# Kernel tuning notes

Hardware: AMD Instinct MI355X
Metric: run time of the kernel (lower is better)

## Reference

```python
import jax, jax.numpy as jnp
import numpy as np

K_HEADS = 8
D_HEAD = 16
D_MODEL = K_HEADS * D_HEAD  # 128


def _xavier(key, shape):
    fan_in, fan_out = shape[0], shape[1]
    limit = (6.0 / (fan_in + fan_out)) ** 0.5
    return jax.random.uniform(key, shape, jnp.float32, -limit, limit)


def setup_inputs() -> dict:
    key = jax.random.key(0)
    ks = jax.random.split(key, 8)
    B, T, N = 8, 12, 512
    X = jax.random.normal(ks[0], (B, T, N, D_MODEL), jnp.float32)
    STE = jax.random.normal(ks[1], (B, T, N, 2 * D_MODEL), jnp.float32)
    Wq = _xavier(ks[2], (3 * D_MODEL, D_MODEL))
    Wk = _xavier(ks[3], (3 * D_MODEL, D_MODEL))
    Wv = _xavier(ks[4], (3 * D_MODEL, D_MODEL))
    Wo = _xavier(ks[5], (D_MODEL, D_MODEL))
    bq = jnp.zeros((D_MODEL,), jnp.float32)
    bk = jnp.zeros((D_MODEL,), jnp.float32)
    bv = jnp.zeros((D_MODEL,), jnp.float32)
    bo = jnp.zeros((D_MODEL,), jnp.float32)
    return {"X": X, "STE": STE, "Wq": Wq, "bq": bq, "Wk": Wk, "bk": bk,
            "Wv": Wv, "bv": bv, "Wo": Wo, "bo": bo}


def reference(X, STE, Wq, bq, Wk, bk, Wv, bv, Wo, bo):
    # 1x1-conv FCs == per-(t,node) linear + relu on the last dim
    H = jnp.concatenate([X, STE], axis=-1)              # [B,T,N,3D]
    q = jax.nn.relu(H @ Wq + bq)                        # [B,T,N,D]
    k = jax.nn.relu(H @ Wk + bk)
    v = jax.nn.relu(H @ Wv + bv)
    B, T, N, D = q.shape

    def heads(x):  # split last dim into K heads (head index major), move to front
        return x.reshape(B, T, N, K_HEADS, D_HEAD).transpose(3, 0, 1, 2, 4)

    qh, kh, vh = heads(q), heads(k), heads(v)           # [K,B,T,N,d]
    att = jnp.einsum('kbtnd,kbtmd->kbtnm', qh, kh) / (D_HEAD ** 0.5)
    att = jax.nn.softmax(att, axis=-1)                  # [K,B,T,N,N]
    o = jnp.einsum('kbtnm,kbtmd->kbtnd', att, vh)       # [K,B,T,N,d]
    o = o.transpose(1, 2, 3, 0, 4).reshape(B, T, N, D)  # concat heads on last dim
    return jax.nn.relu(o @ Wo + bo)
```

## Files before the change

kernel.cpp:

```cpp
#include <hip/hip_runtime.h>
#include <math.h>

constexpr int B_  = 8;
constexpr int T_  = 12;
constexpr int N_  = 512;
constexpr int DM  = 128;
constexpr int KH  = 8;
constexpr int DH  = 16;
constexpr int MR  = B_*T_*N_;
constexpr int K3  = 3*DM;
constexpr int TB  = 256;

typedef __attribute__((ext_vector_type(8))) short  bf16x8;
typedef __attribute__((ext_vector_type(4))) float  f32x4;
typedef __attribute__((ext_vector_type(4))) int    i32x4;

#define LOG2E 1.44269504088896340736f
#define SHIFT2 28.8539008177792681f

static __device__ inline float fast_exp2(float x) {
#if __has_builtin(__builtin_amdgcn_exp2f)
    return __builtin_amdgcn_exp2f(x);
#else
    return __expf(0.69314718055994531f * x);
#endif
}

static __device__ inline unsigned short f2bf(float x) {
    unsigned u = __float_as_uint(x);
    return (unsigned short)((u + 0x7fffu + ((u >> 16) & 1u)) >> 16);
}
static __device__ inline unsigned pk2(float a, float b) {
    unsigned ua = __float_as_uint(a) + 0x8000u;
    unsigned ub = __float_as_uint(b) + 0x8000u;
    return __builtin_amdgcn_perm(ub, ua, 0x07060302u);
}
static __device__ inline unsigned pk2t(float a, float b) {
    return __builtin_amdgcn_perm(__float_as_uint(b), __float_as_uint(a),
                                 0x07060302u);
}
static __device__ inline float fast_rcp(float x) {
#if __has_builtin(__builtin_amdgcn_rcpf)
    return __builtin_amdgcn_rcpf(x);
#else
    return 1.0f / x;
#endif
}

__global__ __launch_bounds__(256) void wprep_kernel(
    const float* __restrict__ Wq, const float* __restrict__ Wk,
    const float* __restrict__ Wv, const float* __restrict__ Wo,
    unsigned short* __restrict__ Wfrag, unsigned short* __restrict__ Wot)
{
    const int idx = blockIdx.x*256 + threadIdx.x;
    if (idx < 3*K3*DM) {
        const int p   = idx / (K3*DM);
        const int rem = idx - p*(K3*DM);
        const int k   = rem >> 7;
        const int n   = rem & 127;
        const float* W = (p == 0) ? Wq : ((p == 1) ? Wk : Wv);
        const int c   = p*DM + n;
        const int nb  = c >> 4, mm = c & 15;
        const int ktI = k >> 6, kr = k & 63;
        const int ksI = kr >> 5, gg = (kr >> 3) & 3, ee = kr & 7;
        Wfrag[(((ktI*24 + nb)*2 + ksI) << 9) + ((gg*16 + mm) << 3) + ee]
            = f2bf(W[rem]);
    } else {
        const int i2 = idx - 3*K3*DM;
        const int k  = i2 >> 7;
        const int n  = i2 & 127;
        Wot[n*DM + k] = f2bf(Wo[i2]);
    }
}

__global__ __launch_bounds__(256, 4) void qkv_fused(
    const float* __restrict__ X, const float* __restrict__ STE,
    const unsigned short* __restrict__ Wfrag,
    const float* __restrict__ bq, const float* __restrict__ bk,
    const float* __restrict__ bv,
    unsigned short* __restrict__ qb, unsigned short* __restrict__ kb2,
    unsigned short* __restrict__ vb2)
{
    __shared__ __align__(16) unsigned short Ash[2][64*72];
    const int tid = threadIdx.x;
    const int rb  = blockIdx.x * 64;
    const int ch  = blockIdx.y;

    const int lane = tid & 63, wv = tid >> 6;
    const int m15 = lane & 15, g = lane >> 4;

    const int ar  = tid >> 4;
    const int ac4 = (tid & 15) * 4;

    float4 a0, a1, a2, a3;

#define QF_LOADA(kt_) {                                                      \
        const float* __restrict__ asrc = ((kt_) < DM) ? (X + (kt_))          \
                                                      : (STE + ((kt_) - DM));\
        const int ldr = ((kt_) < DM) ? DM : 2*DM;                            \
        const float* __restrict__ ap = asrc + (size_t)(rb + ar)*ldr + ac4;   \
        a0 = *(const float4*)(ap           );                                \
        a1 = *(const float4*)(ap + 16*ldr  );                                \
        a2 = *(const float4*)(ap + 32*ldr  );                                \
        a3 = *(const float4*)(ap + 48*ldr  ); }

#define QF_STOREA(buf_) {                                                    \
        unsigned short* Aw = Ash[buf_] + ar*72 + ac4;                        \
        uint2 d;                                                             \
        d.x = pk2(a0.x, a0.y); d.y = pk2(a0.z, a0.w); *(uint2*)(Aw        ) = d; \
        d.x = pk2(a1.x, a1.y); d.y = pk2(a1.z, a1.w); *(uint2*)(Aw + 16*72) = d; \
        d.x = pk2(a2.x, a2.y); d.y = pk2(a2.z, a2.w); *(uint2*)(Aw + 32*72) = d; \
        d.x = pk2(a3.x, a3.y); d.y = pk2(a3.z, a3.w); *(uint2*)(Aw + 48*72) = d; }

    f32x4 acc[4][3] = {};

    const unsigned short* __restrict__ wlane = Wfrag + lane*8;
    const int nb_base = ch*12 + wv*3;

    QF_LOADA(0);
    QF_STOREA(0);

    #pragma unroll
    for (int ktI = 0; ktI < 6; ++ktI) {
        const int cur = ktI & 1;
        __syncthreads();
        if (ktI < 5) { QF_LOADA((ktI + 1) * 64); }
        #pragma unroll
        for (int ksI = 0; ksI < 2; ++ksI) {
            bf16x8 af[4], bfr[3];
            #pragma unroll
            for (int i = 0; i < 4; ++i)
                af[i] = *(const bf16x8*)(Ash[cur] + (i*16 + m15)*72 + ksI*32 + g*8);
            #pragma unroll
            for (int j = 0; j < 3; ++j)
                bfr[j] = *(const bf16x8*)(wlane +
                          (size_t)(((ktI*24 + nb_base + j)*2 + ksI) << 9));
            #pragma unroll
            for (int i = 0; i < 4; ++i)
                #pragma unroll
                for (int j = 0; j < 3; ++j)
                    acc[i][j] = __builtin_amdgcn_mfma_f32_16x16x32_bf16(
                        af[i], bfr[j], acc[i][j], 0, 0, 0);
        }
        if (ktI < 5) { QF_STOREA(cur ^ 1); }
    }

    #pragma unroll
    for (int j = 0; j < 3; ++j) {
        const int c = ch*192 + wv*48 + j*16 + m15;
        const int p = c >> 7;
        const int n = c & 127;
        const float* __restrict__ bias = (p == 0) ? bq : ((p == 1) ? bk : bv);
        unsigned short* __restrict__ outb = (p == 0) ? qb : ((p == 1) ? kb2 : vb2);
        const float scale = (p == 0) ? (0.25f * LOG2E) : 1.0f;
        const float bj = bias[n];
        const int h = n >> 4, d = n & 15;
        #pragma unroll
        for (int i = 0; i < 4; ++i) {
            #pragma unroll
            for (int r = 0; r < 4; ++r) {
                const int row = rb + i*16 + g*4 + r;
                float v = acc[i][j][r] + bj;
                v = (v > 0.f ? v : 0.f) * scale;
                outb[(h*MR + row)*DH + d] = f2bf(v);
            }
        }
    }
}

__global__ __launch_bounds__(256, 4) void attn_kernel(
    const unsigned short* __restrict__ qb, const unsigned short* __restrict__ kb,
    const unsigned short* __restrict__ vb, unsigned short* __restrict__ ob)
{
    __shared__ __align__(16) unsigned short Klds[N_*DH];
    __shared__ __align__(16) unsigned short Vtlds[DH*536];

    const int tid = threadIdx.x;
    const int h   = blockIdx.x & (KH-1);
    const int bt  = blockIdx.x >> 3;
    const int jh  = blockIdx.y;
    const int base = (h*MR + bt*N_) * DH;

    {
        const uint4* kg = (const uint4*)(kb + base);
        uint4* kl = (uint4*)Klds;
        #pragma unroll
        for (int i = 0; i < 4; ++i) kl[tid + i*TB] = kg[tid + i*TB];
    }
    {
        const unsigned* vg = (const unsigned*)(vb + base);
        unsigned a[8], b[8];
        #pragma unroll
        for (int j = 0; j < 8; ++j) {
            a[j] = vg[(2*tid)*8 + j];
            b[j] = vg[(2*tid+1)*8 + j];
        }
        unsigned* vt = (unsigned*)Vtlds;
        #pragma unroll
        for (int d = 0; d < 16; ++d) {
            const int sh = (d & 1) * 16;
            const unsigned lo = (a[d >> 1] >> sh) & 0xffffu;
            const unsigned hi = (b[d >> 1] >> sh) & 0xffffu;
            vt[d*268 + tid] = lo | (hi << 16);
        }
    }
    __syncthreads();

    const int wv   = tid >> 6;
    const int lane = tid & 63;
    const int m    = lane & 15;
    const int g    = lane >> 4;

    bf16x8 qf[4];
    const unsigned short* qp = qb + base + jh*256*DH;
    #pragma unroll
    for (int j = 0; j < 4; ++j) {
        bf16x8 t = {0,0,0,0,0,0,0,0};
        if (g < 2) t = *(const bf16x8*)(qp + ((wv*4 + j)*16 + m)*DH + g*8);
        qf[j] = t;
    }

    const bf16x8 ones = {0x3F80,0x3F80,0x3F80,0x3F80,0x3F80,0x3F80,0x3F80,0x3F80};
    const f32x4 zshift = {-SHIFT2, -SHIFT2, -SHIFT2, -SHIFT2};

    f32x4 acc[4]  = {};
    f32x4 lacc[4] = {};

    for (int c = 0; c < 16; ++c) {
        const int kr0 = c*32 + ((m & 12) << 1) + (m & 3);
        bf16x8 kf0 = {0,0,0,0,0,0,0,0};
        bf16x8 kf1 = {0,0,0,0,0,0,0,0};
        if (g < 2) {
            kf0 = *(const bf16x8*)(Klds + kr0*DH + g*8);
            kf1 = *(const bf16x8*)(Klds + (kr0 + 4)*DH + g*8);
        }
        const bf16x8 vf = *(const bf16x8*)(Vtlds + m*536 + c*32 + g*8);

        #pragma unroll
        for (int j = 0; j < 4; ++j) {
            f32x4 s0 = __builtin_amdgcn_mfma_f32_16x16x32_bf16(kf0, qf[j], zshift, 0, 0, 0);
            f32x4 s1 = __builtin_amdgcn_mfma_f32_16x16x32_bf16(kf1, qf[j], zshift, 0, 0, 0);
            const float p0 = fast_exp2(s0[0]);
            const float p1 = fast_exp2(s0[1]);
            const float p2 = fast_exp2(s0[2]);
            const float p3 = fast_exp2(s0[3]);
            const float p4 = fast_exp2(s1[0]);
            const float p5 = fast_exp2(s1[1]);
            const float p6 = fast_exp2(s1[2]);
            const float p7 = fast_exp2(s1[3]);
            i32x4 pd = { (int)pk2t(p0, p1), (int)pk2t(p2, p3),
                         (int)pk2t(p4, p5), (int)pk2t(p6, p7) };
            const bf16x8 pf = __builtin_bit_cast(bf16x8, pd);
            acc[j]  = __builtin_amdgcn_mfma_f32_16x16x32_bf16(pf, vf,   acc[j],  0, 0, 0);
            lacc[j] = __builtin_amdgcn_mfma_f32_16x16x32_bf16(pf, ones, lacc[j], 0, 0, 0);
        }
    }

    #pragma unroll
    for (int j = 0; j < 4; ++j) {
        #pragma unroll
        for (int r = 0; r < 4; ++r) {
            const float iv = fast_rcp(lacc[j][r]);
            const int qrow = bt*N_ + jh*256 + (wv*4 + j)*16 + 4*g + r;
            ob[qrow*DM + h*DH + m] = f2bf(acc[j][r] * iv);
        }
    }
}

__global__ __launch_bounds__(256, 4) void out_mfma(
    const unsigned short* __restrict__ ot, const unsigned short* __restrict__ Wot,
    const float* __restrict__ bo, float* __restrict__ out)
{
    __shared__ __align__(16) unsigned short Ash[64*136];
    const int tid = threadIdx.x;
    const int rb  = blockIdx.x * 64;
    const int lane = tid & 63, wv = tid >> 6;
    const int m15 = lane & 15, g = lane >> 4;

    #pragma unroll
    for (int i = 0; i < 4; ++i) {
        const int idx = tid + i*TB;
        const int r  = idx >> 4;
        const int kg = idx & 15;
        *(uint4*)(Ash + r*136 + kg*8) = *(const uint4*)(ot + (rb + r)*DM + kg*8);
    }
    __syncthreads();

    f32x4 acc[4][2] = {};
    #pragma unroll
    for (int ks = 0; ks < 128; ks += 32) {
        bf16x8 af[4], bfr[2];
        #pragma unroll
        for (int i = 0; i < 4; ++i)
            af[i] = *(const bf16x8*)(Ash + (i*16 + m15)*136 + ks + g*8);
        #pragma unroll
        for (int j = 0; j < 2; ++j)
            bfr[j] = *(const bf16x8*)(Wot + (wv*32 + j*16 + m15)*DM + ks + g*8);
        #pragma unroll
        for (int i = 0; i < 4; ++i)
            #pragma unroll
            for (int j = 0; j < 2; ++j)
                acc[i][j] = __builtin_amdgcn_mfma_f32_16x16x32_bf16(
                    af[i], bfr[j], acc[i][j], 0, 0, 0);
    }

    #pragma unroll
    for (int j = 0; j < 2; ++j) {
        const int c  = wv*32 + j*16 + m15;
        const float bj = bo[c];
        #pragma unroll
        for (int i = 0; i < 4; ++i) {
            #pragma unroll
            for (int r = 0; r < 4; ++r) {
                const int row = rb + i*16 + g*4 + r;
                float v = acc[i][j][r] + bj;
                out[row*DM + c] = v > 0.f ? v : 0.f;
            }
        }
    }
}

extern "C" void kernel_launch(void* const* d_in, const int* in_sizes, int n_in,
                              void* d_out, int out_size, void* d_ws, size_t ws_size,
                              hipStream_t stream)
{
    const float* X   = (const float*)d_in[0];
    const float* STE = (const float*)d_in[1];
    const float* Wq  = (const float*)d_in[2];
    const float* bq  = (const float*)d_in[3];
    const float* Wk  = (const float*)d_in[4];
    const float* bk  = (const float*)d_in[5];
    const float* Wv  = (const float*)d_in[6];
    const float* bv  = (const float*)d_in[7];
    const float* Wo  = (const float*)d_in[8];
    const float* bo  = (const float*)d_in[9];
    float* out = (float*)d_out;

    unsigned short* qb  = (unsigned short*)d_ws;
    unsigned short* kb  = qb  + (size_t)MR*DM;
    unsigned short* vb  = kb  + (size_t)MR*DM;
    unsigned short* ot  = vb  + (size_t)MR*DM;
    unsigned short* Wt  = ot  + (size_t)MR*DM;
    unsigned short* Wot = Wt  + (size_t)3*K3*DM;

    hipLaunchKernelGGL(wprep_kernel, dim3((3*K3*DM + DM*DM)/TB), dim3(TB), 0, stream,
                       Wq, Wk, Wv, Wo, Wt, Wot);
    hipLaunchKernelGGL(qkv_fused, dim3(MR/64, 2), dim3(TB), 0, stream,
                       X, STE, Wt, bq, bk, bv, qb, kb, vb);
    hipLaunchKernelGGL(attn_kernel, dim3(KH*B_*T_, 2), dim3(TB), 0, stream,
                       qb, kb, vb, ot);
    hipLaunchKernelGGL(out_mfma, dim3(MR/64), dim3(TB), 0, stream,
                       ot, Wot, bo, out);
}
```

Baseline: 183.8 us.

## Retile QKV projection to 32-row blocks covering all 384 output columns

The QKV GEMM kernel now gives each block 32 rows and all 384 output columns, instead of 64 rows over half the columns with a grid split of 2. Each input row of X and STE is therefore read from global memory once rather than twice. The whole 32x384 bf16 A tile is staged into shared memory up front with one barrier, replacing the double-buffered K-loop pipeline. The trade-off is that global loads no longer overlap the MFMAs, shared memory use per block goes up, and each wave now does 6 B-fragment loads for 2 A-fragments, which lowers A reuse per weight load.

```diff
diff --git a/kernel.cpp b/kernel.cpp
--- a/kernel.cpp
+++ b/kernel.cpp
@@ -81,73 +81,80 @@
     unsigned short* __restrict__ qb, unsigned short* __restrict__ kb2,
     unsigned short* __restrict__ vb2)
 {
-    __shared__ __align__(16) unsigned short Ash[2][64*72];
+    __shared__ __align__(16) unsigned short Ash[32*392];
     const int tid = threadIdx.x;
-    const int rb  = blockIdx.x * 64;
-    const int ch  = blockIdx.y;
+    const int rb  = blockIdx.x * 32;
 
     const int lane = tid & 63, wv = tid >> 6;
     const int m15 = lane & 15, g = lane >> 4;
 
-    const int ar  = tid >> 4;
-    const int ac4 = (tid & 15) * 4;
-
-    float4 a0, a1, a2, a3;
-
-#define QF_LOADA(kt_) {                                                      \
-        const float* __restrict__ asrc = ((kt_) < DM) ? (X + (kt_))          \
-                                                      : (STE + ((kt_) - DM));\
-        const int ldr = ((kt_) < DM) ? DM : 2*DM;                            \
-        const float* __restrict__ ap = asrc + (size_t)(rb + ar)*ldr + ac4;   \
-        a0 = *(const float4*)(ap           );                                \
-        a1 = *(const float4*)(ap + 16*ldr  );                                \
-        a2 = *(const float4*)(ap + 32*ldr  );                                \
-        a3 = *(const float4*)(ap + 48*ldr  ); }
-
-#define QF_STOREA(buf_) {                                                    \
-        unsigned short* Aw = Ash[buf_] + ar*72 + ac4;                        \
-        uint2 d;                                                             \
-        d.x = pk2(a0.x, a0.y); d.y = pk2(a0.z, a0.w); *(uint2*)(Aw        ) = d; \
-        d.x = pk2(a1.x, a1.y); d.y = pk2(a1.z, a1.w); *(uint2*)(Aw + 16*72) = d; \
-        d.x = pk2(a2.x, a2.y); d.y = pk2(a2.z, a2.w); *(uint2*)(Aw + 32*72) = d; \
-        d.x = pk2(a3.x, a3.y); d.y = pk2(a3.z, a3.w); *(uint2*)(Aw + 48*72) = d; }
-
-    f32x4 acc[4][3] = {};
-
+    {
+        const int row = tid >> 5;
+        const int c4  = tid & 31;
+        const float* __restrict__ xp = X + (size_t)(rb + row)*DM + c4*4;
+        float4 a0 = *(const float4*)(xp          );
+        float4 a1 = *(const float4*)(xp +  8*DM  );
+        float4 a2 = *(const float4*)(xp + 16*DM  );
+        float4 a3 = *(const float4*)(xp + 24*DM  );
+        unsigned short* Aw = Ash + row*392 + c4*4;
+        uint2 d;
+        d.x = pk2(a0.x, a0.y); d.y = pk2(a0.z, a0.w); *(uint2*)(Aw          ) = d;
+        d.x = pk2(a1.x, a1.y); d.y = pk2(a1.z, a1.w); *(uint2*)(Aw +  8*392) = d;
+        d.x = pk2(a2.x, a2.y); d.y = pk2(a2.z, a2.w); *(uint2*)(Aw + 16*392) = d;
+        d.x = pk2(a3.x, a3.y); d.y = pk2(a3.z, a3.w); *(uint2*)(Aw + 24*392) = d;
+    }
+    {
+        const int row = tid >> 6;
+        const int c4  = tid & 63;
+        const float* __restrict__ ep = STE + (size_t)(rb + row)*(2*DM) + c4*4;
+        float4 e0 = *(const float4*)(ep            );
+        float4 e1 = *(const float4*)(ep +  4*2*DM  );
+        float4 e2 = *(const float4*)(ep +  8*2*DM  );
+        float4 e3 = *(const float4*)(ep + 12*2*DM  );
+        float4 e4 = *(const float4*)(ep + 16*2*DM  );
+        float4 e5 = *(const float4*)(ep + 20*2*DM  );
+        float4 e6 = *(const float4*)(ep + 24*2*DM  );
+        float4 e7 = *(const float4*)(ep + 28*2*DM  );
+        unsigned short* Ew = Ash + row*392 + DM + c4*4;
+        uint2 d;
+        d.x = pk2(e0.x, e0.y); d.y = pk2(e0.z, e0.w); *(uint2*)(Ew          ) = d;
+        d.x = pk2(e1.x, e1.y); d.y = pk2(e1.z, e1.w); *(uint2*)(Ew +  4*392) = d;
+        d.x = pk2(e2.x, e2.y); d.y = pk2(e2.z, e2.w); *(uint2*)(Ew +  8*392) = d;
+        d.x = pk2(e3.x, e3.y); d.y = pk2(e3.z, e3.w); *(uint2*)(Ew + 12*392) = d;
+        d.x = pk2(e4.x, e4.y); d.y = pk2(e4.z, e4.w); *(uint2*)(Ew + 16*392) = d;
+        d.x = pk2(e5.x, e5.y); d.y = pk2(e5.z, e5.w); *(uint2*)(Ew + 20*392) = d;
+        d.x = pk2(e6.x, e6.y); d.y = pk2(e6.z, e6.w); *(uint2*)(Ew + 24*392) = d;
+        d.x = pk2(e7.x, e7.y); d.y = pk2(e7.z, e7.w); *(uint2*)(Ew + 28*392) = d;
+    }
+    __syncthreads();
+
+    f32x4 acc[2][6] = {};
     const unsigned short* __restrict__ wlane = Wfrag + lane*8;
-    const int nb_base = ch*12 + wv*3;
-
-    QF_LOADA(0);
-    QF_STOREA(0);
 
     #pragma unroll
     for (int ktI = 0; ktI < 6; ++ktI) {
-        const int cur = ktI & 1;
-        __syncthreads();
-        if (ktI < 5) { QF_LOADA((ktI + 1) * 64); }
         #pragma unroll
         for (int ksI = 0; ksI < 2; ++ksI) {
-            bf16x8 af[4], bfr[3];
-            #pragma unroll
-            for (int i = 0; i < 4; ++i)
-                af[i] = *(const bf16x8*)(Ash[cur] + (i*16 + m15)*72 + ksI*32 + g*8);
-            #pragma unroll
-            for (int j = 0; j < 3; ++j)
+            bf16x8 af[2], bfr[6];
+            const int kof = ktI*64 + ksI*32 + g*8;
+            af[0] = *(const bf16x8*)(Ash + (     m15)*392 + kof);
+            af[1] = *(const bf16x8*)(Ash + (16 + m15)*392 + kof);
+            #pragma unroll
+            for (int j = 0; j < 6; ++j)
                 bfr[j] = *(const bf16x8*)(wlane +
-                          (size_t)(((ktI*24 + nb_base + j)*2 + ksI) << 9));
-            #pragma unroll
-            for (int i = 0; i < 4; ++i)
+                          (size_t)(((ktI*24 + wv*6 + j)*2 + ksI) << 9));
+            #pragma unroll
+            for (int i = 0; i < 2; ++i)
                 #pragma unroll
-                for (int j = 0; j < 3; ++j)
+                for (int j = 0; j < 6; ++j)
                     acc[i][j] = __builtin_amdgcn_mfma_f32_16x16x32_bf16(
                         af[i], bfr[j], acc[i][j], 0, 0, 0);
         }
-        if (ktI < 5) { QF_STOREA(cur ^ 1); }
-    }
-
-    #pragma unroll
-    for (int j = 0; j < 3; ++j) {
-        const int c = ch*192 + wv*48 + j*16 + m15;
+    }
+
+    #pragma unroll
+    for (int j = 0; j < 6; ++j) {
+        const int c = wv*96 + j*16 + m15;
         const int p = c >> 7;
         const int n = c & 127;
         const float* __restrict__ bias = (p == 0) ? bq : ((p == 1) ? bk : bv);
@@ -156,7 +163,7 @@
         const float bj = bias[n];
         const int h = n >> 4, d = n & 15;
         #pragma unroll
-        for (int i = 0; i < 4; ++i) {
+        for (int i = 0; i < 2; ++i) {
             #pragma unroll
             for (int r = 0; r < 4; ++r) {
                 const int row = rb + i*16 + g*4 + r;
@@ -345,7 +352,7 @@
 
     hipLaunchKernelGGL(wprep_kernel, dim3((3*K3*DM + DM*DM)/TB), dim3(TB), 0, stream,
                        Wq, Wk, Wv, Wo, Wt, Wot);
-    hipLaunchKernelGGL(qkv_fused, dim3(MR/64, 2), dim3(TB), 0, stream,
+    hipLaunchKernelGGL(qkv_fused, dim3(MR/32), dim3(TB), 0, stream,
                        X, STE, Wt, bq, bk, bv, qb, kb, vb);
     hipLaunchKernelGGL(attn_kernel, dim3(KH*B_*T_, 2), dim3(TB), 0, stream,
                        qb, kb, vb, ot);
```

New measurement: 184.2 us. No clear change (+0.2%).
